# Optimization experiments

Hardware: AMD Instinct MI355X
Metric: run time of the kernel (lower is better)

## Reference

```python
import jax, jax.numpy as jnp
import numpy as np

D_MODEL = 192; D_INNER = 384; N_STATE = 16; D_CONV = 4; DT_RANK = 12; DEPTH = 24
PATCH = 16; STRIDE = 16; IMG = 128; EPS = 1e-5


def _ln(x, w, b):
    m = jnp.mean(x, -1, keepdims=True)
    v = jnp.mean((x - m) ** 2, -1, keepdims=True)
    return (x - m) * jax.lax.rsqrt(v + EPS) * w + b


def _mamba_dir(xz, cw, cb, xpw, dpw, dpb, Alog, Dv):
    # xz: (B, L, 2*d_inner); one direction of the bidirectional Mamba mixer
    xp, z = jnp.split(xz, 2, axis=-1)               # (B,L,di) each
    xc = jnp.transpose(xp, (0, 2, 1))               # (B,di,L)
    xc = jnp.pad(xc, ((0, 0), (0, 0), (D_CONV - 1, 0)))  # causal pad
    xc = jax.lax.conv_general_dilated(
        xc, cw, (1,), 'VALID',
        dimension_numbers=('NCH', 'OIH', 'NCH'),
        feature_group_count=D_INNER) + cb[None, :, None]
    u = jax.nn.silu(jnp.transpose(xc, (0, 2, 1)))   # (B,L,di)
    dbl = u @ xpw.T                                  # (B,L,dt_rank+2N)
    dt, Bm, Cm = jnp.split(dbl, [DT_RANK, DT_RANK + N_STATE], axis=-1)
    dt = jax.nn.softplus(dt @ dpw.T + dpb)           # (B,L,di)
    A = -jnp.exp(Alog)                               # (di,N)
    dA = jnp.exp(dt[..., None] * A)                  # (B,L,di,N)
    dBu = (dt * u)[..., None] * Bm[:, :, None, :]    # (B,L,di,N)

    def comb(c1, c2):
        a1, b1 = c1
        a2, b2 = c2
        return a1 * a2, a2 * b1 + b2

    _, h = jax.lax.associative_scan(comb, (dA, dBu), axis=1)
    y = jnp.einsum('bldn,bln->bld', h, Cm) + u * Dv
    return y * jax.nn.silu(z)


def _forward(x, patch_w, patch_b, ln_w, ln_b, in_w,
             cf_w, cf_b, xpf_w, dtf_w, dtf_b, Alog_f, D_f,
             cbk_w, cbk_b, xpb_w, dtb_w, dtb_b, Alog_b, D_b,
             out_w, nf_w, nf_b, head_w, head_b):
    B = x.shape[0]
    p = jax.lax.conv_general_dilated(
        x, patch_w, (STRIDE,) * 3, 'VALID',
        dimension_numbers=('NCDHW', 'OIDHW', 'NCDHW')) + patch_b[None, :, None, None, None]
    hidden = p.reshape(B, D_MODEL, -1).transpose(0, 2, 1)  # (B, L=512, D)
    residual = jnp.zeros_like(hidden)

    xs = (ln_w, ln_b, in_w, cf_w, cf_b, xpf_w, dtf_w, dtf_b, Alog_f, D_f,
          cbk_w, cbk_b, xpb_w, dtb_w, dtb_b, Alog_b, D_b, out_w)

    def step(carry, pl):
        hidden, residual = carry
        (lw, lb, iw, cfw, cfb, xpf, dwf, dbf, Af, Dfv,
         cbw, cbb, xpb, dwb, dbb, Ab, Dbv, ow) = pl
        residual = residual + hidden
        hn = _ln(residual, lw, lb)
        xz = hn @ iw.T                               # (B,L,2di)
        yf = _mamba_dir(xz, cfw, cfb, xpf, dwf, dbf, Af, Dfv)
        yb = jnp.flip(_mamba_dir(jnp.flip(xz, 1), cbw, cbb, xpb, dwb, dbb, Ab, Dbv), 1)
        hidden = (yf + yb) @ ow.T
        return (hidden, residual), None

    (hidden, residual), _ = jax.lax.scan(step, (hidden, residual), xs)
    final = _ln(residual + hidden, nf_w, nf_b)
    feat = final[:, -1, :]                           # final_pool_type='none' -> last token
    return feat @ head_w.T + head_b


def setup_inputs() -> dict:
    key = jax.random.key(0)
    ks = jax.random.split(key, 16)
    rn = lambda k, s, sc=0.02: jax.random.normal(k, s, jnp.float32) * sc
    d = {}
    d['x'] = jax.random.normal(ks[0], (1, 1, IMG, IMG, IMG), jnp.float32)
    d['patch_w'] = rn(ks[1], (D_MODEL, 1, PATCH, PATCH, PATCH), 0.05)
    d['patch_b'] = jnp.zeros((D_MODEL,), jnp.float32)
    d['ln_w'] = jnp.ones((DEPTH, D_MODEL), jnp.float32)
    d['ln_b'] = jnp.zeros((DEPTH, D_MODEL), jnp.float32)
    d['in_w'] = rn(ks[2], (DEPTH, 2 * D_INNER, D_MODEL))
    d['cf_w'] = rn(ks[3], (DEPTH, D_INNER, 1, D_CONV), 0.2)
    d['cf_b'] = jnp.zeros((DEPTH, D_INNER), jnp.float32)
    d['xpf_w'] = rn(ks[4], (DEPTH, DT_RANK + 2 * N_STATE, D_INNER))
    d['dtf_w'] = rn(ks[5], (DEPTH, D_INNER, DT_RANK), 0.1)
    d['dtf_b'] = jnp.full((DEPTH, D_INNER), -4.6, jnp.float32)  # softplus -> dt~0.01
    d['Alog_f'] = jnp.log(jnp.broadcast_to(jnp.arange(1, N_STATE + 1, dtype=jnp.float32), (DEPTH, D_INNER, N_STATE)))
    d['D_f'] = jnp.ones((DEPTH, D_INNER), jnp.float32)
    d['cbk_w'] = rn(ks[6], (DEPTH, D_INNER, 1, D_CONV), 0.2)
    d['cbk_b'] = jnp.zeros((DEPTH, D_INNER), jnp.float32)
    d['xpb_w'] = rn(ks[7], (DEPTH, DT_RANK + 2 * N_STATE, D_INNER))
    d['dtb_w'] = rn(ks[8], (DEPTH, D_INNER, DT_RANK), 0.1)
    d['dtb_b'] = jnp.full((DEPTH, D_INNER), -4.6, jnp.float32)
    d['Alog_b'] = jnp.log(jnp.broadcast_to(jnp.arange(1, N_STATE + 1, dtype=jnp.float32), (DEPTH, D_INNER, N_STATE)))
    d['D_b'] = jnp.ones((DEPTH, D_INNER), jnp.float32)
    d['out_w'] = rn(ks[9], (DEPTH, D_MODEL, D_INNER))
    d['nf_w'] = jnp.ones((D_MODEL,), jnp.float32)
    d['nf_b'] = jnp.zeros((D_MODEL,), jnp.float32)
    d['head_w'] = rn(ks[10], (2, D_MODEL))
    d['head_b'] = jnp.zeros((2,), jnp.float32)
    return d


def reference(x, patch_w, patch_b, ln_w, ln_b, in_w,
              cf_w, cf_b, xpf_w, dtf_w, dtf_b, Alog_f, D_f,
              cbk_w, cbk_b, xpb_w, dtb_w, dtb_b, Alog_b, D_b,
              out_w, nf_w, nf_b, head_w, head_b):
    return _forward(x, patch_w, patch_b, ln_w, ln_b, in_w,
                    cf_w, cf_b, xpf_w, dtf_w, dtf_b, Alog_f, D_f,
                    cbk_w, cbk_b, xpb_w, dtb_w, dtb_b, Alog_b, D_b,
                    out_w, nf_w, nf_b, head_w, head_b)
```

## Files before the change

kernel.cpp:

```cpp
#include <hip/hip_runtime.h>
#include <hip/hip_bf16.h>

#define D_MODEL 192
#define D_INNER 384
#define N_STATE 16
#define DT_RANK 12
#define DEPTH 24
#define SEQ 512
#define NCHUNK 8
#define CLEN 64
#define TS 68
#define AS 33
#define PART_STRIDE (SEQ * D_MODEL)
#define USTR (SEQ * D_INNER)
#define KSPLIT 16
#define NBLK 512
#define FSTR 32
#define XZSTR (SEQ * 2 * D_INNER)
#define CHSTR (2 * NCHUNK * D_INNER * N_STATE)

typedef __hip_bfloat16 bf16;
typedef unsigned short u16;
typedef unsigned long long u64;

__device__ __forceinline__ float silu_f(float x) { return x / (1.f + __expf(-x)); }
__device__ __forceinline__ float softplus_f(float x) {
    return (x > 20.f) ? x : log1pf(__expf(x));
}
__device__ __forceinline__ float bf2f(unsigned u) {
    return __uint_as_float(u << 16);
}
__device__ __forceinline__ u16 f2bu(float f) {
    bf16 b = __float2bfloat16(f);
    return *reinterpret_cast<u16*>(&b);
}

__device__ __forceinline__ float aload(const float* p) {
    return __hip_atomic_load(p, __ATOMIC_RELAXED, __HIP_MEMORY_SCOPE_AGENT);
}
__device__ __forceinline__ void astore(float* p, float v) {
    __hip_atomic_store(p, v, __ATOMIC_RELAXED, __HIP_MEMORY_SCOPE_AGENT);
}
__device__ __forceinline__ unsigned aloadu(const unsigned* p) {
    return __hip_atomic_load(p, __ATOMIC_RELAXED, __HIP_MEMORY_SCOPE_AGENT);
}
__device__ __forceinline__ void astoreu(unsigned* p, unsigned v) {
    __hip_atomic_store(p, v, __ATOMIC_RELAXED, __HIP_MEMORY_SCOPE_AGENT);
}
__device__ __forceinline__ float2 aload2(const float* p) {
    const u64 v = __hip_atomic_load((const u64*)p, __ATOMIC_RELAXED, __HIP_MEMORY_SCOPE_AGENT);
    return make_float2(__uint_as_float((unsigned)v), __uint_as_float((unsigned)(v >> 32)));
}
__device__ __forceinline__ void astore2(float* p, float x, float y) {
    const u64 v = (u64)__float_as_uint(x) | ((u64)__float_as_uint(y) << 32);
    __hip_atomic_store((u64*)p, v, __ATOMIC_RELAXED, __HIP_MEMORY_SCOPE_AGENT);
}
__device__ __forceinline__ float4 aload4v(const float* p) {
    const float2 a = aload2(p), b = aload2(p + 2);
    return make_float4(a.x, a.y, b.x, b.y);
}
__device__ __forceinline__ float4 aload_bf4(const u16* p) {
    const u64 v = __hip_atomic_load((const u64*)p, __ATOMIC_RELAXED, __HIP_MEMORY_SCOPE_AGENT);
    return make_float4(bf2f((unsigned)(v & 0xffffu)),
                       bf2f((unsigned)((v >> 16) & 0xffffu)),
                       bf2f((unsigned)((v >> 32) & 0xffffu)),
                       bf2f((unsigned)(v >> 48)));
}
__device__ __forceinline__ void astore_bf4(u16* p, float a, float b, float c, float d) {
    const u64 v = (u64)f2bu(a) | ((u64)f2bu(b) << 16)
                | ((u64)f2bu(c) << 32) | ((u64)f2bu(d) << 48);
    __hip_atomic_store((u64*)p, v, __ATOMIC_RELAXED, __HIP_MEMORY_SCOPE_AGENT);
}

template<typename T> __device__ __forceinline__ float ld(const void* p, long i) {
    return ((const float*)p)[i];
}
template<> __device__ __forceinline__ float ld<bf16>(const void* p, long i) {
    return bf2f(((const u16*)p)[i]);
}
template<typename T> __device__ __forceinline__ float4 ld4(const void* p, long i) {
    return *(const float4*)((const float*)p + i);
}
template<> __device__ __forceinline__ float4 ld4<bf16>(const void* p, long i) {
    const ushort4 v = *(const ushort4*)((const u16*)p + i);
    return make_float4(bf2f(v.x), bf2f(v.y), bf2f(v.z), bf2f(v.w));
}
template<typename T> __device__ __forceinline__ void st(void* p, int i, float v) {
    ((float*)p)[i] = v;
}
template<> __device__ __forceinline__ void st<bf16>(void* p, int i, float v) {
    ((bf16*)p)[i] = __float2bfloat16(v);
}
__device__ __forceinline__ float dot4(const float4& a, const float4& b) {
    return a.x * b.x + a.y * b.y + a.z * b.z + a.w * b.w;
}
__device__ __forceinline__ void ld8b(const u16* p, float4& a, float4& b) {
    const uint4 u = *(const uint4*)p;
    a.x = bf2f(u.x & 0xffffu); a.y = bf2f(u.x >> 16);
    a.z = bf2f(u.y & 0xffffu); a.w = bf2f(u.y >> 16);
    b.x = bf2f(u.z & 0xffffu); b.y = bf2f(u.z >> 16);
    b.z = bf2f(u.w & 0xffffu); b.w = bf2f(u.w >> 16);
}
__device__ __forceinline__ float4 ld4b(const u16* p) {
    const uint2 u = *(const uint2*)p;
    return make_float4(bf2f(u.x & 0xffffu), bf2f(u.x >> 16),
                       bf2f(u.y & 0xffffu), bf2f(u.y >> 16));
}

__device__ __forceinline__ void post_flag(unsigned* fl, unsigned v, int tid) {
    asm volatile("s_waitcnt vmcnt(0)" ::: "memory");
    __syncthreads();
    if (tid == 0) astoreu(fl, v);
}
__device__ __forceinline__ void wait_flag(const unsigned* fl, unsigned v) {
    int spins = 0;
    while (aloadu(fl) < v) {
        if (++spins > (1 << 20)) break;
        __builtin_amdgcn_s_sleep(1);
    }
}

__device__ __forceinline__ void gbar(unsigned* bar, unsigned target, bool fence) {
    asm volatile("s_waitcnt vmcnt(0)" ::: "memory");
    __syncthreads();
    const int bid = blockIdx.x, tid = threadIdx.x;
    unsigned* gen0 = bar + 512 * FSTR;
    if (tid == 0) {
        if (fence) __threadfence();
        astoreu(&bar[bid * FSTR], target);
    }
    if (bid == 0) {
        int spins = 0;
        for (;;) {
            const unsigned va = aloadu(&bar[tid * FSTR]);
            const unsigned vb = aloadu(&bar[(tid + 256) * FSTR]);
            const bool ok = (va >= target) && (vb >= target);
            if (__syncthreads_and(ok)) break;
            if (++spins > (1 << 20)) break;
            __builtin_amdgcn_s_sleep(1);
        }
        if (tid == 0) astoreu(gen0, target);
    } else if (tid == 0) {
        int spins = 0;
        if (bid < 16) {
            while (aloadu(gen0) < target) {
                if (++spins > (1 << 20)) break;
                __builtin_amdgcn_s_sleep(2);
            }
            astoreu(&gen0[bid * FSTR], target);
        } else if (bid < 32) {
            while (aloadu(gen0) < target) {
                if (++spins > (1 << 20)) break;
                __builtin_amdgcn_s_sleep(2);
            }
        } else {
            unsigned* rl = &gen0[(bid >> 5) * FSTR];
            while (aloadu(rl) < target) {
                if (++spins > (1 << 20)) break;
                __builtin_amdgcn_s_sleep(2);
            }
        }
    }
    if (fence && tid == 0) __threadfence();
    __syncthreads();
}

__device__ void cvtB(const void* s, u16* d, long n, long g, long str, int isb) {
    if (isb) {
        const u16* p = (const u16*)s;
        for (long i = g * 4; i < n; i += str * 4) *(ushort4*)(d + i) = *(const ushort4*)(p + i);
    } else {
        const float* p = (const float*)s;
        for (long i = g * 4; i < n; i += str * 4) {
            const float4 v = *(const float4*)(p + i);
            ushort4 o; o.x = f2bu(v.x); o.y = f2bu(v.y); o.z = f2bu(v.z); o.w = f2bu(v.w);
            *(ushort4*)(d + i) = o;
        }
    }
}
__device__ void cvtF(const void* s, float* d, long n, long g, long str, int isb) {
    if (isb) {
        const u16* p = (const u16*)s;
        for (long i = g * 4; i < n; i += str * 4) {
            const ushort4 v = *(const ushort4*)(p + i);
            *(float4*)(d + i) = make_float4(bf2f(v.x), bf2f(v.y), bf2f(v.z), bf2f(v.w));
        }
    } else {
        const float* p = (const float*)s;
        for (long i = g * 4; i < n; i += str * 4) *(float4*)(d + i) = *(const float4*)(p + i);
    }
}
__device__ void cvtNA(const void* s, float* d, long n, long g, long str, int isb) {
    if (isb) {
        const u16* p = (const u16*)s;
        for (long i = g * 4; i < n; i += str * 4) {
            const ushort4 v = *(const ushort4*)(p + i);
            *(float4*)(d + i) = make_float4(-__expf(bf2f(v.x)), -__expf(bf2f(v.y)),
                                            -__expf(bf2f(v.z)), -__expf(bf2f(v.w)));
        }
    } else {
        const float* p = (const float*)s;
        for (long i = g * 4; i < n; i += str * 4) {
            const float4 v = *(const float4*)(p + i);
            *(float4*)(d + i) = make_float4(-__expf(v.x), -__expf(v.y), -__expf(v.z), -__expf(v.w));
        }
    }
}

template<typename T>
__device__ void final_phase(int tid, const float* res, const u16* yB, const void* ow,
                            const void* nw, const void* nb, const void* hw, const void* hb,
                            void* out, float* syf, float* f, float* red) {
    for (int j = tid; j < 96; j += 256) {
        const int q = j * 4;
        const float4 vf = aload_bf4(&yB[(long)511 * D_INNER + q]);
        const float4 vb = aload_bf4(&yB[(long)USTR + 511 * D_INNER + q]);
        *(float4*)&syf[q] = make_float4(vf.x + vb.x, vf.y + vb.y, vf.z + vb.z, vf.w + vb.w);
    }
    __syncthreads();
    float v = 0.f;
    if (tid < D_MODEL) {
        float acc = 0.f;
        const long wrow = (long)(DEPTH - 1) * D_MODEL * D_INNER + (long)tid * D_INNER;
        for (int k = 0; k < D_INNER; k += 4)
            acc += dot4(ld4<T>(ow, wrow + k), *(const float4*)&syf[k]);
        v = aload(&res[511 * D_MODEL + tid]) + acc;
    }
    float s = v;
    #pragma unroll
    for (int o = 32; o > 0; o >>= 1) s += __shfl_down(s, o, 64);
    if ((tid & 63) == 0 && tid < D_MODEL) red[tid >> 6] = s;
    __syncthreads();
    const float mean = (red[0] + red[1] + red[2]) * (1.f / D_MODEL);
    const float d = (tid < D_MODEL) ? (v - mean) : 0.f;
    float s2 = d * d;
    #pragma unroll
    for (int o = 32; o > 0; o >>= 1) s2 += __shfl_down(s2, o, 64);
    if ((tid & 63) == 0 && tid < D_MODEL) red[3 + (tid >> 6)] = s2;
    __syncthreads();
    const float var = (red[3] + red[4] + red[5]) * (1.f / D_MODEL);
    if (tid < D_MODEL)
        f[tid] = d * rsqrtf(var + 1e-5f) * ld<T>(nw, tid) + ld<T>(nb, tid);
    __syncthreads();
    if (tid < 2) {
        float a2 = ld<T>(hb, tid);
        for (int c = 0; c < D_MODEL; ++c) a2 += f[c] * ld<T>(hw, tid * D_MODEL + c);
        st<T>(out, tid, a2);
    }
}

struct MegaArgs {
    const void *x, *pw, *pb, *lnw, *lnb, *inw, *cfw, *cfb, *xpfw, *dtfw, *dtfb, *Af, *Dfv;
    const void *cbw, *cbb, *xpbw, *dtbw, *dtbb, *Ab, *Dbv, *ow, *nfw, *nfb, *hw, *hb;
    void* out;
    unsigned* bar;
    float *hidC, *res0, *res1, *dbl, *dt, *chunkH, *chunkP;
    u16 *xzB, *uB, *yB;
    float *lnwF, *lnbF, *cbfF, *cbbF, *dtbfF, *dtbbF, *negAfF, *negAbF, *DfF, *DbF, *pbF;
    u16 *inwB, *owB, *xB, *pwB, *xpwfB, *xpwbB, *dtwfB, *dtwbB, *cwfB, *cwbB;
};

__global__ void init_kernel(unsigned* bar) {
    const int i = blockIdx.x * 256 + threadIdx.x;
    ((uint4*)bar)[i] = make_uint4(0, 0, 0, 0);
}

__global__ void __launch_bounds__(256, 2) mega_kernel(MegaArgs a) {
    __shared__ float smem[6144];
    const int bid = blockIdx.x;
    const int tid = threadIdx.x;
    unsigned* bar = a.bar;
    unsigned* scanR = a.bar + 528 * FSTR;
    unsigned* aflag = a.bar + 912 * FSTR;
    unsigned* bflag = a.bar + 1168 * FSTR;
    unsigned* yflag = a.bar + 1680 * FSTR;
    unsigned gen_ctr = 0;
    const int isb = (((const unsigned*)a.lnw)[0] != 0x3F800000u);

    {
        const long g = (long)bid * 256 + tid;
        const long str = (long)NBLK * 256;
        cvtB(a.inw,  a.inwB,  3538944, g, str, isb);
        cvtB(a.ow,   a.owB,   1769472, g, str, isb);
        cvtB(a.x,    a.xB,    2097152, g, str, isb);
        cvtB(a.pw,   a.pwB,    786432, g, str, isb);
        cvtB(a.xpfw, a.xpwfB,  405504, g, str, isb);
        cvtB(a.xpbw, a.xpwbB,  405504, g, str, isb);
        cvtB(a.dtfw, a.dtwfB,  110592, g, str, isb);
        cvtB(a.dtbw, a.dtwbB,  110592, g, str, isb);
        cvtB(a.cfw,  a.cwfB,    36864, g, str, isb);
        cvtB(a.cbw,  a.cwbB,    36864, g, str, isb);
        cvtF(a.lnw,  a.lnwF,     4608, g, str, isb);
        cvtF(a.lnb,  a.lnbF,     4608, g, str, isb);
        cvtF(a.cfb,  a.cbfF,     9216, g, str, isb);
        cvtF(a.cbb,  a.cbbF,     9216, g, str, isb);
        cvtF(a.dtfb, a.dtbfF,    9216, g, str, isb);
        cvtF(a.dtbb, a.dtbbF,    9216, g, str, isb);
        cvtF(a.pb,   a.pbF,       192, g, str, isb);
        cvtNA(a.Af,  a.negAfF,  147456, g, str, isb);
        cvtNA(a.Ab,  a.negAbF,  147456, g, str, isb);
        cvtF(a.Dfv,  a.DfF,      9216, g, str, isb);
        cvtF(a.Dbv,  a.DbF,      9216, g, str, isb);
    }
    gbar(bar, ++gen_ctr, true);

    {
        float* As_ = smem;
        float* Ws  = smem + 1056;
        const int ty = tid >> 4, tx = tid & 15;
        for (int unit = bid; unit < 768; unit += NBLK) {
            const int mt = unit & 15, nt = (unit >> 4) % 3, ks = unit / 48;
            const int m0 = mt * 32, n0 = nt * 64, kk0 = ks * 256;
            float acc[2][4] = {};
            for (int kk = kk0; kk < kk0 + 256; kk += 32) {
                for (int e = tid; e < 1024; e += 256) {
                    const int m = e >> 5, k = e & 31;
                    const int kid = kk + k, t = m0 + m;
                    const int dz = kid >> 8, dy = (kid >> 4) & 15, dx = kid & 15;
                    const int pz = t >> 6, py = (t >> 3) & 7, px = t & 7;
                    As_[k * AS + m] = bf2f(a.xB[(long)(pz * 16 + dz) * 16384 + (py * 16 + dy) * 128 + (px * 16 + dx)]);
                }
                for (int e = tid; e < 2048; e += 256) {
                    const int n = e >> 5, k = e & 31;
                    Ws[k * TS + n] = bf2f(a.pwB[(long)(n0 + n) * 4096 + kk + k]);
                }
                __syncthreads();
                #pragma unroll 8
                for (int k = 0; k < 32; ++k) {
                    const float a0 = As_[k * AS + ty * 2];
                    const float a1 = As_[k * AS + ty * 2 + 1];
                    const float4 w4 = *(const float4*)&Ws[k * TS + tx * 4];
                    acc[0][0] += a0 * w4.x; acc[0][1] += a0 * w4.y;
                    acc[0][2] += a0 * w4.z; acc[0][3] += a0 * w4.w;
                    acc[1][0] += a1 * w4.x; acc[1][1] += a1 * w4.y;
                    acc[1][2] += a1 * w4.z; acc[1][3] += a1 * w4.w;
                }
                __syncthreads();
            }
            float* C = a.hidC + (long)ks * PART_STRIDE;
            #pragma unroll
            for (int i = 0; i < 2; ++i) {
                float4 o4 = make_float4(acc[i][0], acc[i][1], acc[i][2], acc[i][3]);
                if (ks == 0) {
                    o4.x += a.pbF[n0 + tx * 4 + 0];
                    o4.y += a.pbF[n0 + tx * 4 + 1];
                    o4.z += a.pbF[n0 + tx * 4 + 2];
                    o4.w += a.pbF[n0 + tx * 4 + 3];
                }
                astore2(&C[(m0 + ty * 2 + i) * D_MODEL + n0 + tx * 4], o4.x, o4.y);
                astore2(&C[(m0 + ty * 2 + i) * D_MODEL + n0 + tx * 4 + 2], o4.z, o4.w);
            }
        }
    }
    gbar(bar, ++gen_ctr, false);

    const int ch = tid >> 4, np = tid & 15;
    float* sU  = smem;
    float* sDT = smem + 1024;
    float* sBC = smem + 2048;
    float* sZ  = smem + 4096;
    float* sY  = smem + 5120;

    for (int l = 0; l < DEPTH; ++l) {
        const int first = (l == 0);
        const unsigned lv = (unsigned)(l + 1);
        const int par = l & 1;
        u16* xzP = a.xzB + (long)par * XZSTR;
        u16* uP  = a.uB  + (long)par * (2 * USTR);
        float* dtP = a.dt + (long)par * (2 * USTR);
        float* dbG = a.dbl + (long)par * (2 * SEQ * 44);
        float* chH = a.chunkH + (long)par * CHSTR;
        float* chPb = a.chunkP + (long)par * CHSTR;
        const float* resIn = par ? a.res1 : a.res0;
        float* resOut      = par ? a.res0 : a.res1;

        if (bid < 256) {
            if (par) {
                if (tid < 48) {
                    const int dd = tid / 24, dg = tid - dd * 24;
                    const int cf = bid >> 5;
                    const int cb = (511 - 2 * bid) >> 6;
                    const int cc = dd ? cb : cf;
                    wait_flag(&yflag[((dd * NCHUNK + cc) * 24 + dg) * FSTR], (unsigned)l);
                }
                __syncthreads();
            }
            float* sy  = smem;
            float* lnS = smem + 768;
            float* hnS = smem + 1152;
            float* xzS = smem + 1536;
            const int t0 = bid * 2;
            if (!first) {
                for (int j = tid; j < 192; j += 256) {
                    const int tt = j / 96, q4 = (j - tt * 96) * 4;
                    const long o = (long)(t0 + tt) * D_INNER + q4;
                    const float4 vf = aload_bf4(&a.yB[o]);
                    const float4 vb = aload_bf4(&a.yB[(long)USTR + o]);
                    *(float4*)&sy[tt * D_INNER + q4] =
                        make_float4(vf.x + vb.x, vf.y + vb.y, vf.z + vb.z, vf.w + vb.w);
                }
            }
            __syncthreads();
            if (tid < D_MODEL) {
                float accB[2];
                if (first) {
                    #pragma unroll
                    for (int tt = 0; tt < 2; ++tt) {
                        float s = 0.f;
                        #pragma unroll
                        for (int sp = 0; sp < KSPLIT; ++sp)
                            s += aload(&a.hidC[(long)sp * PART_STRIDE + (t0 + tt) * D_MODEL + tid]);
                        accB[tt] = s;
                    }
                } else {
                    accB[0] = accB[1] = 0.f;
                    const u16* wr = a.owB + (long)(l - 1) * D_MODEL * D_INNER + (long)tid * D_INNER;
                    for (int k = 0; k < D_INNER; k += 8) {
                        float4 va, vb;
                        ld8b(wr + k, va, vb);
                        accB[0] += dot4(va, *(const float4*)&sy[k]) + dot4(vb, *(const float4*)&sy[k + 4]);
                        accB[1] += dot4(va, *(const float4*)&sy[D_INNER + k]) + dot4(vb, *(const float4*)&sy[D_INNER + k + 4]);
                    }
                }
                #pragma unroll
                for (int tt = 0; tt < 2; ++tt) {
                    const float rv = accB[tt] + (first ? 0.f : aload(&resIn[(t0 + tt) * D_MODEL + tid]));
                    lnS[tt * D_MODEL + tid] = rv;
                    astore(&resOut[(t0 + tt) * D_MODEL + tid], rv);
                }
            }
            __syncthreads();
            {
                const int w = tid >> 6, lane = tid & 63;
                if (w < 2) {
                    const float v0 = lnS[w * D_MODEL + lane];
                    const float v1 = lnS[w * D_MODEL + lane + 64];
                    const float v2 = lnS[w * D_MODEL + lane + 128];
                    float s = v0 + v1 + v2;
                    #pragma unroll
                    for (int o = 32; o > 0; o >>= 1) s += __shfl_xor(s, o, 64);
                    const float mean = s * (1.f / D_MODEL);
                    const float d0 = v0 - mean, d1 = v1 - mean, d2 = v2 - mean;
                    float s2 = d0 * d0 + d1 * d1 + d2 * d2;
                    #pragma unroll
                    for (int o = 32; o > 0; o >>= 1) s2 += __shfl_xor(s2, o, 64);
                    const float rstd = rsqrtf(s2 * (1.f / D_MODEL) + 1e-5f);
                    hnS[w * D_MODEL + lane]       = d0 * rstd * a.lnwF[l * D_MODEL + lane]       + a.lnbF[l * D_MODEL + lane];
                    hnS[w * D_MODEL + lane + 64]  = d1 * rstd * a.lnwF[l * D_MODEL + lane + 64]  + a.lnbF[l * D_MODEL + lane + 64];
                    hnS[w * D_MODEL + lane + 128] = d2 * rstd * a.lnwF[l * D_MODEL + lane + 128] + a.lnbF[l * D_MODEL + lane + 128];
                }
            }
            __syncthreads();
            float accD[3][2] = {};
            const u16* w0 = a.inwB + (long)l * 2 * D_INNER * D_MODEL;
            for (int k = 0; k < D_MODEL; k += 8) {
                #pragma unroll
                for (int r = 0; r < 3; ++r) {
                    float4 va, vb;
                    ld8b(w0 + (long)(tid + r * 256) * D_MODEL + k, va, vb);
                    #pragma unroll
                    for (int tt = 0; tt < 2; ++tt) {
                        accD[r][tt] += dot4(va, *(const float4*)&hnS[tt * D_MODEL + k])
                                     + dot4(vb, *(const float4*)&hnS[tt * D_MODEL + k + 4]);
                    }
                }
            }
            #pragma unroll
            for (int r = 0; r < 3; ++r)
                #pragma unroll
                for (int tt = 0; tt < 2; ++tt)
                    xzS[tt * 768 + tid + r * 256] = accD[r][tt];
            __syncthreads();
            for (int j = tid; j < 384; j += 256) {
                const int tok = j / 192, q = (j - tok * 192) * 4;
                const float* s = &xzS[tok * 768 + q];
                astore_bf4(&xzP[(long)(t0 + tok) * 2 * D_INNER + q], s[0], s[1], s[2], s[3]);
            }
            post_flag(&aflag[bid * FSTR], lv, tid);
        }

        {
            const int dir = bid >> 8, bb = bid & 255;
            int lo, hi;
            if (dir == 0) { lo = bb >= 2 ? bb - 2 : 0; hi = bb; }
            else { lo = bb <= 255 ? (255 - bb > 0 ? 255 - bb : 0) : 0;
                   hi = 257 - bb <= 255 ? 257 - bb : 255; }
            if (tid <= hi - lo) wait_flag(&aflag[(lo + tid) * FSTR], lv);
            __syncthreads();

            float* su   = smem;
            float* dblP = smem + 768;
            float* dblS = smem + 960;
            const u16* cwB   = dir ? a.cwbB  : a.cwfB;
            const float* cbF = dir ? a.cbbF  : a.cbfF;
            const u16* xpwB  = dir ? a.xpwbB : a.xpwfB;
            const u16* dtwB  = dir ? a.dtwbB : a.dtwfB;
            const float* dtbF = dir ? a.dtbbF : a.dtbfF;
            const int t0 = bb * 2;
            u16* ub = uP + (long)dir * USTR;
            for (int j = tid; j < 192; j += 256) {
                const int tt = j / 96, q4 = (j - tt * 96) * 4;
                const int t = t0 + tt;
                float4 wA, wB2, wC, wD;
                ld8b(cwB + (long)(l * D_INNER + q4) * 4, wA, wB2);
                ld8b(cwB + (long)(l * D_INNER + q4) * 4 + 8, wC, wD);
                const float cw0[4] = {wA.x, wA.y, wA.z, wA.w};
                const float cw1[4] = {wB2.x, wB2.y, wB2.z, wB2.w};
                const float cw2[4] = {wC.x, wC.y, wC.z, wC.w};
                const float cw3[4] = {wD.x, wD.y, wD.z, wD.w};
                float4 acc = *(const float4*)&cbF[l * D_INNER + q4];
                #pragma unroll
                for (int k = 0; k < 4; ++k) {
                    const int ii = t + k - 3;
                    if (ii >= 0) {
                        const int src = dir ? (511 - ii) : ii;
                        const float4 xq = aload_bf4(&xzP[(long)src * 2 * D_INNER + q4]);
                        acc.x += xq.x * cw0[k]; acc.y += xq.y * cw1[k];
                        acc.z += xq.z * cw2[k]; acc.w += xq.w * cw3[k];
                    }
                }
                const float u0 = silu_f(acc.x), u1 = silu_f(acc.y);
                const float u2 = silu_f(acc.z), u3 = silu_f(acc.w);
                *(float4*)&su[tt * D_INNER + q4] = make_float4(u0, u1, u2, u3);
                astore_bf4(&ub[(long)t * D_INNER + q4], u0, u1, u2, u3);
            }
            __syncthreads();
            if (tid < 176) {
                const int half = tid / 88;
                const int r = tid - half * 88;
                const int tt = r / 44, out = r - tt * 44;
                const u16* wr = xpwB + (long)(l * 44 + out) * D_INNER;
                const int k0 = half * 192;
                float acc = 0.f;
                for (int k = k0; k < k0 + 192; k += 8) {
                    float4 va, vb;
                    ld8b(wr + k, va, vb);
                    acc += dot4(va, *(const float4*)&su[tt * D_INNER + k])
                         + dot4(vb, *(const float4*)&su[tt * D_INNER + k + 4]);
                }
                dblP[half * 96 + tt * 48 + out] = acc;
            }
            __syncthreads();
            if (tid < 88) {
                const int tt = tid / 44, out = tid - tt * 44;
                const float s = dblP[tt * 48 + out] + dblP[96 + tt * 48 + out];
                dblS[tt * 48 + out] = s;
                astore(&dbG[(long)dir * SEQ * 44 + (long)(t0 + tt) * 44 + out], s);
            }
            __syncthreads();
            float* dtp = dtP + (long)dir * USTR;
            for (int j = tid; j < 384; j += 256) {
                const int tt = j / 192, d2 = (j - tt * 192) * 2;
                const u16* wr = dtwB + (long)(l * D_INNER + d2) * DT_RANK;
                float4 A0, B0; ld8b(wr, A0, B0);
                const float4 C0 = ld4b(wr + 8);
                float4 A1, B1; ld8b(wr + 12, A1, B1);
                const float4 C1 = ld4b(wr + 20);
                const float* ds = &dblS[tt * 48];
                const float4 ds0 = *(const float4*)ds;
                const float4 ds1 = *(const float4*)(ds + 4);
                const float4 ds2 = *(const float4*)(ds + 8);
                const float acc0 = dtbF[l * D_INNER + d2]
                    + dot4(A0, ds0) + dot4(B0, ds1) + dot4(C0, ds2);
                const float acc1 = dtbF[l * D_INNER + d2 + 1]
                    + dot4(A1, ds0) + dot4(B1, ds1) + dot4(C1, ds2);
                astore2(&dtp[(long)(t0 + tt) * D_INNER + d2],
                        softplus_f(acc0), softplus_f(acc1));
            }
            post_flag(&bflag[bid * FSTR], lv, tid);
        }

        if (bid < 384) {
            const int dg = bid % 24, chunk = (bid / 24) & 7, dir2 = bid / 192;
            if (tid < 32) wait_flag(&bflag[(dir2 * 256 + chunk * 32 + tid) * FSTR], lv);
            __syncthreads();
            const int d0 = dg * 16, d = d0 + ch;
            const int t0s = chunk * CLEN;
            const u16* ubq  = uP + (long)dir2 * USTR;
            const float* dtp = dtP + (long)dir2 * USTR;
            const float* db  = dbG + (long)dir2 * SEQ * 44;
            {
                const int t = tid >> 2, dl4 = (tid & 3) * 4;
                const int tg = t0s + t;
                const long base = (long)tg * D_INNER + d0 + dl4;
                *(float4*)&sU[t * 16 + dl4]  = aload_bf4(&ubq[base]);
                *(float4*)&sDT[t * 16 + dl4] = aload4v(&dtp[base]);
                const int out_l = dir2 ? (511 - tg) : tg;
                *(float4*)&sZ[t * 16 + dl4] = aload_bf4(&xzP[(long)out_l * 2 * D_INNER + D_INNER + d0 + dl4]);
            }
            for (int i = tid; i < 512; i += 256) {
                const int t = i >> 3, j4 = (i & 7) * 4;
                *(float4*)&sBC[t * 32 + j4] = aload4v(&db[(long)(t0s + t) * 44 + DT_RANK + j4]);
            }
            const float* negA = dir2 ? a.negAbF : a.negAfF;
            const float Areg = negA[(long)(l * D_INNER + d) * N_STATE + np];
            const float Dval = (dir2 ? a.DbF : a.DfF)[l * D_INNER + d];
            __syncthreads();
            float h = 0.f, dts = 0.f;
            for (int t = 0; t < CLEN; ++t) {
                const float dtv = sDT[t * 16 + ch];
                h = __expf(dtv * Areg) * h + (dtv * sU[t * 16 + ch]) * sBC[t * 32 + np];
                dts += dtv;
            }
            const long cb2 = ((long)(dir2 * NCHUNK + chunk) * D_INNER + d) * N_STATE + np;
            astore(&chH[cb2], h);
            astore(&chPb[cb2], __expf(Areg * dts));
            post_flag(&scanR[((dir2 * NCHUNK + chunk) * 24 + dg) * FSTR], lv, tid);
            if (tid < chunk) wait_flag(&scanR[((dir2 * NCHUNK + tid) * 24 + dg) * FSTR], lv);
            __syncthreads();
            float hs[NCHUNK - 1], ps[NCHUNK - 1];
            #pragma unroll
            for (int c = 0; c < NCHUNK - 1; ++c) {
                if (c < chunk) {
                    const long cbb = ((long)(dir2 * NCHUNK + c) * D_INNER + d) * N_STATE + np;
                    hs[c] = aload(&chH[cbb]);
                    ps[c] = aload(&chPb[cbb]);
                }
            }
            float h0 = 0.f;
            #pragma unroll
            for (int c = 0; c < NCHUNK - 1; ++c)
                if (c < chunk) h0 = ps[c] * h0 + hs[c];
            h = h0;
            for (int t = 0; t < CLEN; ++t) {
                const float dtv = sDT[t * 16 + ch];
                const float uv = sU[t * 16 + ch];
                h = __expf(dtv * Areg) * h + (dtv * uv) * sBC[t * 32 + np];
                float part = h * sBC[t * 32 + 16 + np];
                part += __shfl_xor(part, 1, 64);
                part += __shfl_xor(part, 2, 64);
                part += __shfl_xor(part, 4, 64);
                part += __shfl_xor(part, 8, 64);
                if (np == 0)
                    sY[t * 16 + ch] = (part + uv * Dval) * silu_f(sZ[t * 16 + ch]);
            }
            __syncthreads();
            {
                const int t = tid >> 2, dl4 = (tid & 3) * 4;
                const int tg = t0s + t;
                const int out_l = dir2 ? (511 - tg) : tg;
                u16* yb = a.yB + (long)dir2 * USTR;
                const float* s = &sY[t * 16 + dl4];
                astore_bf4(&yb[(long)out_l * D_INNER + d0 + dl4], s[0], s[1], s[2], s[3]);
            }
            post_flag(&yflag[((dir2 * NCHUNK + chunk) * 24 + dg) * FSTR], lv, tid);
        }
        if (par) gbar(bar, ++gen_ctr, false);
    }

    if (bid == 0) {
        float* syf = smem;
        float* f   = smem + 384;
        float* red = smem + 576;
        if (isb) final_phase<bf16>(tid, a.res0, a.yB, a.ow, a.nfw, a.nfb, a.hw, a.hb, a.out, syf, f, red);
        else     final_phase<float>(tid, a.res0, a.yB, a.ow, a.nfw, a.nfb, a.hw, a.hb, a.out, syf, f, red);
    }
}

extern "C" void kernel_launch(void* const* d_in, const int* in_sizes, int n_in,
                              void* d_out, int out_size, void* d_ws, size_t ws_size,
                              hipStream_t stream) {
    (void)in_sizes; (void)n_in; (void)out_size; (void)ws_size;
    const void* x    = d_in[0];
    const void* pw   = d_in[1];
    const void* pb   = d_in[2];
    const void* lnw  = d_in[3];
    const void* lnb  = d_in[4];
    const void* inw  = d_in[5];
    const void* cfw  = d_in[6];
    const void* cfb  = d_in[7];
    const void* xpfw = d_in[8];
    const void* dtfw = d_in[9];
    const void* dtfb = d_in[10];
    const void* Af   = d_in[11];
    const void* Dfv  = d_in[12];
    const void* cbw  = d_in[13];
    const void* cbb  = d_in[14];
    const void* xpbw = d_in[15];
    const void* dtbw = d_in[16];
    const void* dtbb = d_in[17];
    const void* Ab   = d_in[18];
    const void* Dbv  = d_in[19];
    const void* ow   = d_in[20];
    const void* nfw  = d_in[21];
    const void* nfb  = d_in[22];
    const void* hw   = d_in[23];
    const void* hb   = d_in[24];

    unsigned* bar = (unsigned*)d_ws;
    float* w = (float*)((char*)d_ws + 327680);
    float* hidC   = w;  w += KSPLIT * PART_STRIDE;
    float* res0   = w;  w += PART_STRIDE;
    float* res1   = w;  w += PART_STRIDE;
    float* dbl    = w;  w += 2 * 2 * SEQ * 44;
    float* dt     = w;  w += 2 * 2 * USTR;
    float* chunkH = w;  w += 2 * CHSTR;
    float* chunkP = w;  w += 2 * CHSTR;
    float* lnwF = w;  w += 4608;
    float* lnbF = w;  w += 4608;
    float* cbfF = w;  w += 9216;
    float* cbbF = w;  w += 9216;
    float* dtbfF = w; w += 9216;
    float* dtbbF = w; w += 9216;
    float* negAfF = w; w += 147456;
    float* negAbF = w; w += 147456;
    float* DfF = w;   w += 9216;
    float* DbF = w;   w += 9216;
    float* pbF = w;   w += 192;
    u16* b = (u16*)w;
    u16* xzB = b;  b += 2 * XZSTR;
    u16* uB  = b;  b += 2 * 2 * USTR;
    u16* yB  = b;  b += 2 * USTR;
    u16* inwB  = b;  b += 3538944;
    u16* owB   = b;  b += 1769472;
    u16* xB    = b;  b += 2097152;
    u16* pwB   = b;  b += 786432;
    u16* xpwfB = b;  b += 405504;
    u16* xpwbB = b;  b += 405504;
    u16* dtwfB = b;  b += 110592;
    u16* dtwbB = b;  b += 110592;
    u16* cwfB  = b;  b += 36864;
    u16* cwbB  = b;  b += 36864;

    MegaArgs ma;
    ma.x = x; ma.pw = pw; ma.pb = pb; ma.lnw = lnw; ma.lnb = lnb; ma.inw = inw;
    ma.cfw = cfw; ma.cfb = cfb; ma.xpfw = xpfw; ma.dtfw = dtfw; ma.dtfb = dtfb;
    ma.Af = Af; ma.Dfv = Dfv; ma.cbw = cbw; ma.cbb = cbb; ma.xpbw = xpbw;
    ma.dtbw = dtbw; ma.dtbb = dtbb; ma.Ab = Ab; ma.Dbv = Dbv; ma.ow = ow;
    ma.nfw = nfw; ma.nfb = nfb; ma.hw = hw; ma.hb = hb; ma.out = d_out;
    ma.bar = bar;
    ma.hidC = hidC; ma.res0 = res0; ma.res1 = res1; ma.dbl = dbl; ma.dt = dt;
    ma.chunkH = chunkH; ma.chunkP = chunkP;
    ma.xzB = xzB; ma.uB = uB; ma.yB = yB;
    ma.lnwF = lnwF; ma.lnbF = lnbF; ma.cbfF = cbfF; ma.cbbF = cbbF;
    ma.dtbfF = dtbfF; ma.dtbbF = dtbbF; ma.negAfF = negAfF; ma.negAbF = negAbF;
    ma.DfF = DfF; ma.DbF = DbF; ma.pbF = pbF;
    ma.inwB = inwB; ma.owB = owB; ma.xB = xB; ma.pwB = pwB;
    ma.xpwfB = xpwfB; ma.xpwbB = xpwbB; ma.dtwfB = dtwfB; ma.dtwbB = dtwbB;
    ma.cwfB = cwfB; ma.cwbB = cwbB;

    init_kernel<<<80, 256, 0, stream>>>(bar);
    mega_kernel<<<NBLK, 256, 0, stream>>>(ma);
}
```

Baseline: 1.886 ms.

## Double persistent grid to 1024 blocks, one token per block in per-token stages

Raises the persistent mega-kernel grid from 512 to 1024 blocks with four blocks per CU, and reworks the LN/in-projection and conv/x-proj/dt stages so each block handles one token instead of two. The grid barrier, flag layout and workspace offsets are resized to match, and the scan stage now waits on 64 per-token flags. The aim is more parallelism and latency hiding in the per-token GEMV stages. In exchange each weight row is reused for only one token, so weight traffic per token doubles, and the higher launch bound tightens the register budget. Barrier cost also grows with twice as many blocks, and all 1024 blocks must be co-resident for the spin barriers to work.

```diff
diff --git a/kernel.cpp b/kernel.cpp
--- a/kernel.cpp
+++ b/kernel.cpp
@@ -14,10 +14,15 @@
 #define PART_STRIDE (SEQ * D_MODEL)
 #define USTR (SEQ * D_INNER)
 #define KSPLIT 16
-#define NBLK 512
+#define NBLK 1024
 #define FSTR 32
 #define XZSTR (SEQ * 2 * D_INNER)
 #define CHSTR (2 * NCHUNK * D_INNER * N_STATE)
+#define GEN_OFF   1024
+#define SCANR_OFF 1056
+#define AFLAG_OFF 1440
+#define BFLAG_OFF 1952
+#define YFLAG_OFF 2976
 
 typedef __hip_bfloat16 bf16;
 typedef unsigned short u16;
@@ -124,7 +129,7 @@
     asm volatile("s_waitcnt vmcnt(0)" ::: "memory");
     __syncthreads();
     const int bid = blockIdx.x, tid = threadIdx.x;
-    unsigned* gen0 = bar + 512 * FSTR;
+    unsigned* gen0 = bar + GEN_OFF * FSTR;
     if (tid == 0) {
         if (fence) __threadfence();
         astoreu(&bar[bid * FSTR], target);
@@ -134,7 +139,9 @@
         for (;;) {
             const unsigned va = aloadu(&bar[tid * FSTR]);
             const unsigned vb = aloadu(&bar[(tid + 256) * FSTR]);
-            const bool ok = (va >= target) && (vb >= target);
+            const unsigned vc = aloadu(&bar[(tid + 512) * FSTR]);
+            const unsigned vd = aloadu(&bar[(tid + 768) * FSTR]);
+            const bool ok = (va >= target) && (vb >= target) && (vc >= target) && (vd >= target);
             if (__syncthreads_and(ok)) break;
             if (++spins > (1 << 20)) break;
             __builtin_amdgcn_s_sleep(1);
@@ -142,17 +149,12 @@
         if (tid == 0) astoreu(gen0, target);
     } else if (tid == 0) {
         int spins = 0;
-        if (bid < 16) {
+        if (bid < 32) {
             while (aloadu(gen0) < target) {
                 if (++spins > (1 << 20)) break;
                 __builtin_amdgcn_s_sleep(2);
             }
             astoreu(&gen0[bid * FSTR], target);
-        } else if (bid < 32) {
-            while (aloadu(gen0) < target) {
-                if (++spins > (1 << 20)) break;
-                __builtin_amdgcn_s_sleep(2);
-            }
         } else {
             unsigned* rl = &gen0[(bid >> 5) * FSTR];
             while (aloadu(rl) < target) {
@@ -265,15 +267,15 @@
     ((uint4*)bar)[i] = make_uint4(0, 0, 0, 0);
 }
 
-__global__ void __launch_bounds__(256, 2) mega_kernel(MegaArgs a) {
+__global__ void __launch_bounds__(256, 4) mega_kernel(MegaArgs a) {
     __shared__ float smem[6144];
     const int bid = blockIdx.x;
     const int tid = threadIdx.x;
     unsigned* bar = a.bar;
-    unsigned* scanR = a.bar + 528 * FSTR;
-    unsigned* aflag = a.bar + 912 * FSTR;
-    unsigned* bflag = a.bar + 1168 * FSTR;
-    unsigned* yflag = a.bar + 1680 * FSTR;
+    unsigned* scanR = a.bar + SCANR_OFF * FSTR;
+    unsigned* aflag = a.bar + AFLAG_OFF * FSTR;
+    unsigned* bflag = a.bar + BFLAG_OFF * FSTR;
+    unsigned* yflag = a.bar + YFLAG_OFF * FSTR;
     unsigned gen_ctr = 0;
     const int isb = (((const unsigned*)a.lnw)[0] != 0x3F800000u);
 
@@ -304,11 +306,12 @@
     }
     gbar(bar, ++gen_ctr, true);
 
-    {
+    if (bid < 768) {
         float* As_ = smem;
         float* Ws  = smem + 1056;
         const int ty = tid >> 4, tx = tid & 15;
-        for (int unit = bid; unit < 768; unit += NBLK) {
+        const int unit = bid;
+        {
             const int mt = unit & 15, nt = (unit >> 4) % 3, ks = unit / 48;
             const int m0 = mt * 32, n0 = nt * 64, kk0 = ks * 256;
             float acc[2][4] = {};
@@ -374,68 +377,58 @@
         const float* resIn = par ? a.res1 : a.res0;
         float* resOut      = par ? a.res0 : a.res1;
 
-        if (bid < 256) {
+        if (bid < 512) {
+            const int t = bid;
             if (par) {
                 if (tid < 48) {
                     const int dd = tid / 24, dg = tid - dd * 24;
-                    const int cf = bid >> 5;
-                    const int cb = (511 - 2 * bid) >> 6;
-                    const int cc = dd ? cb : cf;
+                    const int cf = t >> 6;
+                    const int cbk = (511 - t) >> 6;
+                    const int cc = dd ? cbk : cf;
                     wait_flag(&yflag[((dd * NCHUNK + cc) * 24 + dg) * FSTR], (unsigned)l);
                 }
                 __syncthreads();
             }
             float* sy  = smem;
-            float* lnS = smem + 768;
-            float* hnS = smem + 1152;
-            float* xzS = smem + 1536;
-            const int t0 = bid * 2;
-            if (!first) {
-                for (int j = tid; j < 192; j += 256) {
-                    const int tt = j / 96, q4 = (j - tt * 96) * 4;
-                    const long o = (long)(t0 + tt) * D_INNER + q4;
-                    const float4 vf = aload_bf4(&a.yB[o]);
-                    const float4 vb = aload_bf4(&a.yB[(long)USTR + o]);
-                    *(float4*)&sy[tt * D_INNER + q4] =
-                        make_float4(vf.x + vb.x, vf.y + vb.y, vf.z + vb.z, vf.w + vb.w);
-                }
+            float* lnS = smem + 384;
+            float* hnS = smem + 576;
+            float* xzS = smem + 768;
+            if (!first && tid < 96) {
+                const int q4 = tid * 4;
+                const long o = (long)t * D_INNER + q4;
+                const float4 vf = aload_bf4(&a.yB[o]);
+                const float4 vb = aload_bf4(&a.yB[(long)USTR + o]);
+                *(float4*)&sy[q4] = make_float4(vf.x + vb.x, vf.y + vb.y, vf.z + vb.z, vf.w + vb.w);
             }
             __syncthreads();
             if (tid < D_MODEL) {
-                float accB[2];
+                float acc;
                 if (first) {
+                    float s = 0.f;
                     #pragma unroll
-                    for (int tt = 0; tt < 2; ++tt) {
-                        float s = 0.f;
-                        #pragma unroll
-                        for (int sp = 0; sp < KSPLIT; ++sp)
-                            s += aload(&a.hidC[(long)sp * PART_STRIDE + (t0 + tt) * D_MODEL + tid]);
-                        accB[tt] = s;
-                    }
+                    for (int sp = 0; sp < KSPLIT; ++sp)
+                        s += aload(&a.hidC[(long)sp * PART_STRIDE + t * D_MODEL + tid]);
+                    acc = s;
                 } else {
-                    accB[0] = accB[1] = 0.f;
+                    acc = 0.f;
                     const u16* wr = a.owB + (long)(l - 1) * D_MODEL * D_INNER + (long)tid * D_INNER;
                     for (int k = 0; k < D_INNER; k += 8) {
                         float4 va, vb;
                         ld8b(wr + k, va, vb);
-                        accB[0] += dot4(va, *(const float4*)&sy[k]) + dot4(vb, *(const float4*)&sy[k + 4]);
-                        accB[1] += dot4(va, *(const float4*)&sy[D_INNER + k]) + dot4(vb, *(const float4*)&sy[D_INNER + k + 4]);
+                        acc += dot4(va, *(const float4*)&sy[k]) + dot4(vb, *(const float4*)&sy[k + 4]);
                     }
                 }
-                #pragma unroll
-                for (int tt = 0; tt < 2; ++tt) {
-                    const float rv = accB[tt] + (first ? 0.f : aload(&resIn[(t0 + tt) * D_MODEL + tid]));
-                    lnS[tt * D_MODEL + tid] = rv;
-                    astore(&resOut[(t0 + tt) * D_MODEL + tid], rv);
-                }
+                const float rv = acc + (first ? 0.f : aload(&resIn[t * D_MODEL + tid]));
+                lnS[tid] = rv;
+                astore(&resOut[t * D_MODEL + tid], rv);
             }
             __syncthreads();
             {
                 const int w = tid >> 6, lane = tid & 63;
-                if (w < 2) {
-                    const float v0 = lnS[w * D_MODEL + lane];
-                    const float v1 = lnS[w * D_MODEL + lane + 64];
-                    const float v2 = lnS[w * D_MODEL + lane + 128];
+                if (w == 0) {
+                    const float v0 = lnS[lane];
+                    const float v1 = lnS[lane + 64];
+                    const float v2 = lnS[lane + 128];
                     float s = v0 + v1 + v2;
                     #pragma unroll
                     for (int o = 32; o > 0; o >>= 1) s += __shfl_xor(s, o, 64);
@@ -445,62 +438,53 @@
                     #pragma unroll
                     for (int o = 32; o > 0; o >>= 1) s2 += __shfl_xor(s2, o, 64);
                     const float rstd = rsqrtf(s2 * (1.f / D_MODEL) + 1e-5f);
-                    hnS[w * D_MODEL + lane]       = d0 * rstd * a.lnwF[l * D_MODEL + lane]       + a.lnbF[l * D_MODEL + lane];
-                    hnS[w * D_MODEL + lane + 64]  = d1 * rstd * a.lnwF[l * D_MODEL + lane + 64]  + a.lnbF[l * D_MODEL + lane + 64];
-                    hnS[w * D_MODEL + lane + 128] = d2 * rstd * a.lnwF[l * D_MODEL + lane + 128] + a.lnbF[l * D_MODEL + lane + 128];
-                }
-            }
-            __syncthreads();
-            float accD[3][2] = {};
+                    hnS[lane]       = d0 * rstd * a.lnwF[l * D_MODEL + lane]       + a.lnbF[l * D_MODEL + lane];
+                    hnS[lane + 64]  = d1 * rstd * a.lnwF[l * D_MODEL + lane + 64]  + a.lnbF[l * D_MODEL + lane + 64];
+                    hnS[lane + 128] = d2 * rstd * a.lnwF[l * D_MODEL + lane + 128] + a.lnbF[l * D_MODEL + lane + 128];
+                }
+            }
+            __syncthreads();
+            float accD[3] = {};
             const u16* w0 = a.inwB + (long)l * 2 * D_INNER * D_MODEL;
             for (int k = 0; k < D_MODEL; k += 8) {
                 #pragma unroll
                 for (int r = 0; r < 3; ++r) {
                     float4 va, vb;
                     ld8b(w0 + (long)(tid + r * 256) * D_MODEL + k, va, vb);
-                    #pragma unroll
-                    for (int tt = 0; tt < 2; ++tt) {
-                        accD[r][tt] += dot4(va, *(const float4*)&hnS[tt * D_MODEL + k])
-                                     + dot4(vb, *(const float4*)&hnS[tt * D_MODEL + k + 4]);
-                    }
+                    accD[r] += dot4(va, *(const float4*)&hnS[k])
+                             + dot4(vb, *(const float4*)&hnS[k + 4]);
                 }
             }
             #pragma unroll
-            for (int r = 0; r < 3; ++r)
-                #pragma unroll
-                for (int tt = 0; tt < 2; ++tt)
-                    xzS[tt * 768 + tid + r * 256] = accD[r][tt];
-            __syncthreads();
-            for (int j = tid; j < 384; j += 256) {
-                const int tok = j / 192, q = (j - tok * 192) * 4;
-                const float* s = &xzS[tok * 768 + q];
-                astore_bf4(&xzP[(long)(t0 + tok) * 2 * D_INNER + q], s[0], s[1], s[2], s[3]);
-            }
-            post_flag(&aflag[bid * FSTR], lv, tid);
+            for (int r = 0; r < 3; ++r) xzS[tid + r * 256] = accD[r];
+            __syncthreads();
+            if (tid < 192) {
+                const int q = tid * 4;
+                const float* s = &xzS[q];
+                astore_bf4(&xzP[(long)t * 2 * D_INNER + q], s[0], s[1], s[2], s[3]);
+            }
+            post_flag(&aflag[t * FSTR], lv, tid);
         }
 
         {
-            const int dir = bid >> 8, bb = bid & 255;
+            const int dir = bid >> 9, t = bid & 511;
             int lo, hi;
-            if (dir == 0) { lo = bb >= 2 ? bb - 2 : 0; hi = bb; }
-            else { lo = bb <= 255 ? (255 - bb > 0 ? 255 - bb : 0) : 0;
-                   hi = 257 - bb <= 255 ? 257 - bb : 255; }
+            if (dir == 0) { lo = t >= 3 ? t - 3 : 0; hi = t; }
+            else { lo = 508 - t >= 0 ? 508 - t : 0; hi = 511 - t; }
             if (tid <= hi - lo) wait_flag(&aflag[(lo + tid) * FSTR], lv);
             __syncthreads();
 
             float* su   = smem;
-            float* dblP = smem + 768;
-            float* dblS = smem + 960;
+            float* dblP = smem + 384;
+            float* dblS = smem + 472;
             const u16* cwB   = dir ? a.cwbB  : a.cwfB;
             const float* cbF = dir ? a.cbbF  : a.cbfF;
             const u16* xpwB  = dir ? a.xpwbB : a.xpwfB;
             const u16* dtwB  = dir ? a.dtwbB : a.dtwfB;
             const float* dtbF = dir ? a.dtbbF : a.dtbfF;
-            const int t0 = bb * 2;
             u16* ub = uP + (long)dir * USTR;
-            for (int j = tid; j < 192; j += 256) {
-                const int tt = j / 96, q4 = (j - tt * 96) * 4;
-                const int t = t0 + tt;
+            if (tid < 96) {
+                const int q4 = tid * 4;
                 float4 wA, wB2, wC, wD;
                 ld8b(cwB + (long)(l * D_INNER + q4) * 4, wA, wB2);
                 ld8b(cwB + (long)(l * D_INNER + q4) * 4 + 8, wC, wD);
@@ -521,61 +505,55 @@
                 }
                 const float u0 = silu_f(acc.x), u1 = silu_f(acc.y);
                 const float u2 = silu_f(acc.z), u3 = silu_f(acc.w);
-                *(float4*)&su[tt * D_INNER + q4] = make_float4(u0, u1, u2, u3);
+                *(float4*)&su[q4] = make_float4(u0, u1, u2, u3);
                 astore_bf4(&ub[(long)t * D_INNER + q4], u0, u1, u2, u3);
             }
             __syncthreads();
-            if (tid < 176) {
-                const int half = tid / 88;
-                const int r = tid - half * 88;
-                const int tt = r / 44, out = r - tt * 44;
+            if (tid < 88) {
+                const int half = tid / 44, out = tid - half * 44;
                 const u16* wr = xpwB + (long)(l * 44 + out) * D_INNER;
                 const int k0 = half * 192;
                 float acc = 0.f;
                 for (int k = k0; k < k0 + 192; k += 8) {
                     float4 va, vb;
                     ld8b(wr + k, va, vb);
-                    acc += dot4(va, *(const float4*)&su[tt * D_INNER + k])
-                         + dot4(vb, *(const float4*)&su[tt * D_INNER + k + 4]);
-                }
-                dblP[half * 96 + tt * 48 + out] = acc;
-            }
-            __syncthreads();
-            if (tid < 88) {
-                const int tt = tid / 44, out = tid - tt * 44;
-                const float s = dblP[tt * 48 + out] + dblP[96 + tt * 48 + out];
-                dblS[tt * 48 + out] = s;
-                astore(&dbG[(long)dir * SEQ * 44 + (long)(t0 + tt) * 44 + out], s);
+                    acc += dot4(va, *(const float4*)&su[k]) + dot4(vb, *(const float4*)&su[k + 4]);
+                }
+                dblP[half * 44 + out] = acc;
+            }
+            __syncthreads();
+            if (tid < 44) {
+                const float s = dblP[tid] + dblP[44 + tid];
+                dblS[tid] = s;
+                astore(&dbG[(long)dir * SEQ * 44 + (long)t * 44 + tid], s);
             }
             __syncthreads();
             float* dtp = dtP + (long)dir * USTR;
-            for (int j = tid; j < 384; j += 256) {
-                const int tt = j / 192, d2 = (j - tt * 192) * 2;
+            if (tid < 192) {
+                const int d2 = tid * 2;
                 const u16* wr = dtwB + (long)(l * D_INNER + d2) * DT_RANK;
                 float4 A0, B0; ld8b(wr, A0, B0);
                 const float4 C0 = ld4b(wr + 8);
                 float4 A1, B1; ld8b(wr + 12, A1, B1);
                 const float4 C1 = ld4b(wr + 20);
-                const float* ds = &dblS[tt * 48];
-                const float4 ds0 = *(const float4*)ds;
-                const float4 ds1 = *(const float4*)(ds + 4);
-                const float4 ds2 = *(const float4*)(ds + 8);
+                const float4 ds0 = *(const float4*)&dblS[0];
+                const float4 ds1 = *(const float4*)&dblS[4];
+                const float4 ds2 = *(const float4*)&dblS[8];
                 const float acc0 = dtbF[l * D_INNER + d2]
                     + dot4(A0, ds0) + dot4(B0, ds1) + dot4(C0, ds2);
                 const float acc1 = dtbF[l * D_INNER + d2 + 1]
                     + dot4(A1, ds0) + dot4(B1, ds1) + dot4(C1, ds2);
-                astore2(&dtp[(long)(t0 + tt) * D_INNER + d2],
-                        softplus_f(acc0), softplus_f(acc1));
+                astore2(&dtp[(long)t * D_INNER + d2], softplus_f(acc0), softplus_f(acc1));
             }
             post_flag(&bflag[bid * FSTR], lv, tid);
         }
 
         if (bid < 384) {
             const int dg = bid % 24, chunk = (bid / 24) & 7, dir2 = bid / 192;
-            if (tid < 32) wait_flag(&bflag[(dir2 * 256 + chunk * 32 + tid) * FSTR], lv);
+            const int t0s = chunk * CLEN;
+            if (tid < 64) wait_flag(&bflag[(dir2 * 512 + t0s + tid) * FSTR], lv);
             __syncthreads();
             const int d0 = dg * 16, d = d0 + ch;
-            const int t0s = chunk * CLEN;
             const u16* ubq  = uP + (long)dir2 * USTR;
             const float* dtp = dtP + (long)dir2 * USTR;
             const float* db  = dbG + (long)dir2 * SEQ * 44;
@@ -688,7 +666,7 @@
     const void* hb   = d_in[24];
 
     unsigned* bar = (unsigned*)d_ws;
-    float* w = (float*)((char*)d_ws + 327680);
+    float* w = (float*)((char*)d_ws + 524288);
     float* hidC   = w;  w += KSPLIT * PART_STRIDE;
     float* res0   = w;  w += PART_STRIDE;
     float* res1   = w;  w += PART_STRIDE;
@@ -739,6 +717,6 @@
     ma.xpwfB = xpwfB; ma.xpwbB = xpwbB; ma.dtwfB = dtwfB; ma.dtwbB = dtwbB;
     ma.cwfB = cwfB; ma.cwbB = cwbB;
 
-    init_kernel<<<80, 256, 0, stream>>>(bar);
+    init_kernel<<<128, 256, 0, stream>>>(bar);
     mega_kernel<<<NBLK, 256, 0, stream>>>(ma);
 }
```

Result: faster. 1.817 ms (-3.7%).
